# Performance work log

Measured on AMD Instinct MI355X. Metric: run time of the kernel, lower is better.

## Reference

```python
import math
import jax, jax.numpy as jnp
import numpy as np

D_MODEL = 1024
NUM_HEADS = 16
D_K = D_MODEL // NUM_HEADS
RANK = 16
B, L = 2, 2048


def setup_inputs() -> dict:
    key = jax.random.key(0)
    ks = jax.random.split(key, 10)
    w_scale = 0.02  # keep activations well-scaled like trained linears
    return {
        "x_q": jax.random.normal(ks[0], (B, L, D_MODEL), jnp.float32),
        "x_kv": jax.random.normal(ks[1], (B, L, D_MODEL), jnp.float32),
        "Wq": jax.random.normal(ks[2], (D_MODEL, D_MODEL), jnp.float32) * w_scale,
        "bq": jnp.zeros((D_MODEL,), jnp.float32),
        "Wk": jax.random.normal(ks[3], (D_MODEL, D_MODEL), jnp.float32) * w_scale,
        "bk": jnp.zeros((D_MODEL,), jnp.float32),
        "Wv": jax.random.normal(ks[4], (D_MODEL, D_MODEL), jnp.float32) * w_scale,
        "bv": jnp.zeros((D_MODEL,), jnp.float32),
        "Wo": jax.random.normal(ks[5], (D_MODEL, D_MODEL), jnp.float32) * w_scale,
        "bo": jnp.zeros((D_MODEL,), jnp.float32),
        "U_bil": jax.random.normal(ks[6], (NUM_HEADS, D_K, RANK), jnp.float32) * 0.02,
        "V_bil": jax.random.normal(ks[7], (NUM_HEADS, D_K, RANK), jnp.float32) * 0.02,
        "padding_mask": jnp.zeros((B, L), bool),  # True = padded KV position
    }


def reference(x_q, x_kv, Wq, bq, Wk, bk, Wv, bv, Wo, bo, U_bil, V_bil, padding_mask):
    b, l, _ = x_q.shape
    # torch nn.Linear: y = x @ W.T + b
    Q = (x_q @ Wq.T + bq).reshape(b, l, NUM_HEADS, D_K).transpose(0, 2, 1, 3)  # [B,H,L,dk]
    K = (x_kv @ Wk.T + bk).reshape(b, l, NUM_HEADS, D_K).transpose(0, 2, 1, 3)
    V = (x_kv @ Wv.T + bv).reshape(b, l, NUM_HEADS, D_K).transpose(0, 2, 1, 3)
    # low-rank bilinear projections: [B,H,L,rank]
    Q_proj = jnp.einsum("bhld,hdr->bhlr", Q, U_bil)
    K_proj = jnp.einsum("bhld,hdr->bhlr", K, V_bil)
    scores = jnp.einsum("bhqr,bhkr->bhqk", Q_proj, K_proj) / math.sqrt(RANK)  # [B,H,L,L]
    scores = jnp.where(padding_mask[:, None, None, :], jnp.float32(-10000.0), scores)
    attn = jax.nn.softmax(scores, axis=-1)  # dropout is identity in eval mode
    ctx = jnp.einsum("bhqk,bhkd->bhqd", attn, V)
    ctx = ctx.transpose(0, 2, 1, 3).reshape(b, l, D_MODEL)
    return ctx @ Wo.T + bo
```

## Files before the change

kernel.cpp:

```cpp
#include <hip/hip_runtime.h>
#include <hip/hip_bf16.h>

#define DM   1024
#define NH   16
#define DK   64
#define RK   16
#define BB   2
#define LL   2048
#define TT   (BB*LL)
#define HRK  256
#define NSPL 2


typedef float f4   __attribute__((ext_vector_type(4)));
typedef float f16v __attribute__((ext_vector_type(16)));
typedef short s8v  __attribute__((ext_vector_type(8)));
typedef unsigned int u2v __attribute__((ext_vector_type(2)));
typedef unsigned int u4v __attribute__((ext_vector_type(4)));

static __device__ __forceinline__ unsigned short f2b(float f) {
  __hip_bfloat16 h = __float2bfloat16(f);
  unsigned short u;
  __builtin_memcpy(&u, &h, 2);
  return u;
}
static __device__ __forceinline__ float b2f(unsigned short u) {
  __hip_bfloat16 h;
  __builtin_memcpy(&h, &u, 2);
  return __bfloat162float(h);
}

__global__ __launch_bounds__(256) void cast_all(
    const float* __restrict__ s0, unsigned short* __restrict__ d0, int n0,
    const float* __restrict__ s1, unsigned short* __restrict__ d1, int n1,
    const float* __restrict__ s2, unsigned short* __restrict__ d2, int n2,
    const float* __restrict__ s3, unsigned short* __restrict__ d3, int n3) {
  const float* s; unsigned short* d; int n;
  switch (blockIdx.y) {
    case 0:  s = s0; d = d0; n = n0; break;
    case 1:  s = s1; d = d1; n = n1; break;
    case 2:  s = s2; d = d2; n = n2; break;
    default: s = s3; d = d3; n = n3; break;
  }
  for (int i = blockIdx.x*256 + threadIdx.x; i < n; i += gridDim.x*256) {
    const float4 v = ((const float4*)s)[i];
    ushort4 o;
    o.x = f2b(v.x); o.y = f2b(v.y); o.z = f2b(v.z); o.w = f2b(v.w);
    ((ushort4*)d)[i] = o;
  }
}

__global__ __launch_bounds__(256) void fuse_w(
    const float* __restrict__ Wq, const float* __restrict__ Wk,
    const float* __restrict__ Uq, const float* __restrict__ Uk,
    unsigned short* __restrict__ Aq, unsigned short* __restrict__ Ak) {
  const float* W = blockIdx.z ? Wk : Wq;
  const float* U = blockIdx.z ? Uk : Uq;
  unsigned short* At = blockIdx.z ? Ak : Aq;
  __shared__ float Us[64][16];
  __shared__ float Ws[4][64];
  const int i0 = blockIdx.x * 64;
  const int h  = blockIdx.y;
  const int tid = threadIdx.x;
  const int il = tid & 63, rr = tid >> 6;
  for (int t = tid; t < 64*16; t += 256)
    Us[t >> 4][t & 15] = U[(size_t)(h*DK + (t >> 4))*RK + (t & 15)];
  float acc[4] = {};
  for (int d0 = 0; d0 < DK; d0 += 4) {
    __syncthreads();
    Ws[rr][il] = W[(size_t)(h*DK + d0 + rr)*DM + i0 + il];
    __syncthreads();
#pragma unroll
    for (int dd = 0; dd < 4; ++dd) {
      const float w = Ws[dd][il];
#pragma unroll
      for (int j = 0; j < 4; ++j)
        acc[j] += w * Us[d0 + dd][rr*4 + j];
    }
  }
#pragma unroll
  for (int j = 0; j < 4; ++j)
    At[(size_t)(h*RK + rr*4 + j)*DM + i0 + il] = f2b(acc[j]);
}

__global__ void bias2(const float* __restrict__ bq, const float* __restrict__ bk,
                      const float* __restrict__ Uq, const float* __restrict__ Uk,
                      float* __restrict__ bpq, float* __restrict__ bpk) {
  const int t = threadIdx.x;
  const float* b = (t < 256) ? bq : bk;
  const float* U = (t < 256) ? Uq : Uk;
  float* bp = (t < 256) ? bpq : bpk;
  const int hr = t & 255, h = hr >> 4, r = hr & 15;
  float acc = 0.f;
  for (int d = 0; d < DK; ++d)
    acc += b[h*DK + d] * U[(size_t)(h*DK + d)*RK + r];
  bp[hr] = acc;
}

__global__ __launch_bounds__(256) void vsum_k(
    const unsigned short* __restrict__ Vt, float* __restrict__ Vsum) {
  const int h = blockIdx.x, b = blockIdx.y;
  const int d = threadIdx.x >> 2, part = threadIdx.x & 3;
  const unsigned short* row = Vt + ((size_t)b*DM + h*DK + d)*LL + part*512;
  float s = 0.f;
  for (int i = 0; i < 512; i += 8) {
    const s8v v = *(const s8v*)&row[i];
#pragma unroll
    for (int j = 0; j < 8; ++j) s += b2f((unsigned short)v[j]);
  }
  s += __shfl_xor(s, 1);
  s += __shfl_xor(s, 2);
  if (part == 0) Vsum[((size_t)b*NH + h)*DK + d] = s;
}

template<int N_, int MODE, int AF32>
__global__ __launch_bounds__(256) void gemm64(
    const void* __restrict__ A0, const void* __restrict__ A1,
    const unsigned short* __restrict__ B0, const unsigned short* __restrict__ B1,
    const float* __restrict__ bi0, const float* __restrict__ bi1,
    void* __restrict__ C0, void* __restrict__ C1) {
  const void* Agv = blockIdx.z ? A1 : A0;
  const unsigned short* Bg = blockIdx.z ? B1 : B0;
  const float* bias = blockIdx.z ? bi1 : bi0;
  void* Cgv = blockIdx.z ? C1 : C0;
  __shared__ unsigned short Xs[64*40];
  __shared__ unsigned short Bs[128*40];
  const int t0 = blockIdx.x * 64, n0 = blockIdx.y * 128;
  const int tid = threadIdx.x, wave = tid >> 6, lane = tid & 63;
  const int quad = lane >> 4, l15 = lane & 15;
  const int nh = wave * 32;

  const f4 z = {0.f, 0.f, 0.f, 0.f};
  f4 acc[4][2];
#pragma unroll
  for (int a = 0; a < 4; ++a) { acc[a][0] = z; acc[a][1] = z; }

  for (int k0 = 0; k0 < DM; k0 += 32) {
    __syncthreads();
    {
      const int ar = tid >> 2, ap = tid & 3;
      if (AF32) {
        const float* Af = (const float*)Agv;
        const float4 x0 = *(const float4*)&Af[(size_t)(t0 + ar)*DM + k0 + ap*8];
        const float4 x1 = *(const float4*)&Af[(size_t)(t0 + ar)*DM + k0 + ap*8 + 4];
        s8v v;
        v[0]=(short)f2b(x0.x); v[1]=(short)f2b(x0.y);
        v[2]=(short)f2b(x0.z); v[3]=(short)f2b(x0.w);
        v[4]=(short)f2b(x1.x); v[5]=(short)f2b(x1.y);
        v[6]=(short)f2b(x1.z); v[7]=(short)f2b(x1.w);
        *(s8v*)&Xs[ar*40 + ap*8] = v;
      } else {
        *(s8v*)&Xs[ar*40 + ap*8] =
            *(const s8v*)&((const unsigned short*)Agv)[(size_t)(t0 + ar)*DM + k0 + ap*8];
      }
      const int br = tid >> 1, bp = tid & 1;
      *(s8v*)&Bs[br*40 + bp*16] =
          *(const s8v*)&Bg[(size_t)(n0 + br)*DM + k0 + bp*16];
      *(s8v*)&Bs[br*40 + bp*16 + 8] =
          *(const s8v*)&Bg[(size_t)(n0 + br)*DM + k0 + bp*16 + 8];
    }
    __syncthreads();

    s8v af[4], bf[2];
#pragma unroll
    for (int ms = 0; ms < 4; ++ms)
      af[ms] = *(const s8v*)&Xs[(ms*16 + l15)*40 + quad*8];
#pragma unroll
    for (int ns = 0; ns < 2; ++ns)
      bf[ns] = *(const s8v*)&Bs[(nh + ns*16 + l15)*40 + quad*8];
#pragma unroll
    for (int ms = 0; ms < 4; ++ms)
#pragma unroll
      for (int ns = 0; ns < 2; ++ns)
        acc[ms][ns] = __builtin_amdgcn_mfma_f32_16x16x32_bf16(
            af[ms], bf[ns], acc[ms][ns], 0, 0, 0);
  }

#pragma unroll
  for (int ms = 0; ms < 4; ++ms) {
    const int tb = t0 + ms*16 + quad*4;
#pragma unroll
    for (int ns = 0; ns < 2; ++ns) {
      const int o = n0 + nh + ns*16 + l15;
      const float bv = bias[o];
      f4 a = acc[ms][ns];
      if (MODE == 0) {
        float* C = (float*)Cgv;
#pragma unroll
        for (int rg = 0; rg < 4; ++rg)
          C[(size_t)(tb + rg)*N_ + o] = a[rg] + bv;
      } else if (MODE == 1) {
        unsigned short* C = (unsigned short*)Cgv;
#pragma unroll
        for (int rg = 0; rg < 4; ++rg) {
          const int tt = tb + rg;
          C[(((size_t)(tt >> 11)*NH + (o >> 4))*LL + (tt & 2047))*RK + (o & 15)]
              = f2b(a[rg] + bv);
        }
      } else {
        unsigned short* C = (unsigned short*)Cgv;
        const int bb = tb >> 11, l = tb & 2047;
        ushort4 pk;
        pk.x = f2b(a[0] + bv); pk.y = f2b(a[1] + bv);
        pk.z = f2b(a[2] + bv); pk.w = f2b(a[3] + bv);
        *(ushort4*)&C[((size_t)bb*DM + o)*LL + l] = pk;
      }
    }
  }
}

template<bool MASKED>
static __device__ __forceinline__ void softmax_pack(
    const f16v& s0, const f16v& s1, const unsigned long long mb, const int hi,
    float& den, unsigned int (&Pd)[2][4][2]) {
#pragma unroll
  for (int nt = 0; nt < 2; ++nt) {
    const f16v& sv = nt ? s1 : s0;
#pragma unroll
    for (int r = 0; r < 4; ++r) {
      float ep[4];
#pragma unroll
      for (int j = 0; j < 4; ++j) {
        float em = __expf(sv[r*4 + j] * 0.25f);
        if (MASKED) {
          const int kloc = nt*32 + j + 8*r + 4*hi;
          if ((mb >> kloc) & 1ull) em = 0.f;
        }
        den += em;
        ep[j] = em - 1.f;
      }
      asm("v_cvt_pk_bf16_f32 %0, %1, %2"
          : "=v"(Pd[nt][r][0]) : "v"(ep[0]), "v"(ep[1]));
      asm("v_cvt_pk_bf16_f32 %0, %1, %2"
          : "=v"(Pd[nt][r][1]) : "v"(ep[2]), "v"(ep[3]));
    }
  }
}

__global__ __launch_bounds__(256) void attention_v8(
    const unsigned short* __restrict__ Qp, const unsigned short* __restrict__ Kp,
    const unsigned short* __restrict__ Vt,
    const unsigned char* __restrict__ msk,
    unsigned short* __restrict__ P, float* __restrict__ denP) {
  __shared__ __align__(16) unsigned short Ks[2][2][64][8];
  __shared__ __align__(16) unsigned short Vs[2][8][64][8];
  const int q0 = blockIdx.x * 128, h = blockIdx.y;
  const int b = blockIdx.z & (BB - 1), ksp = blockIdx.z >> 1;
  const int kbeg = ksp * (LL / NSPL);
  const int NT = (LL / NSPL) / 64;
  const int tid = threadIdx.x, w = tid >> 6, lane = tid & 63;
  const int l31 = lane & 31, hi = lane >> 5;

  const s8v qfrag = *(const s8v*)&Qp[
      (((size_t)b*NH + h)*LL + q0 + w*32 + l31)*RK + hi*8];

  const int sr = tid >> 2, sp = tid & 3;
  const unsigned short* __restrict__ Vrow =
      Vt + ((size_t)b*DM + h*DK + sr)*LL + kbeg;
  const unsigned short* __restrict__ Kbase =
      Kp + (((size_t)b*NH + h)*LL + kbeg + sr)*RK + sp*4;
  const unsigned char*  __restrict__ Mrow = msk + (size_t)b*LL + kbeg + lane;

  u2v kpre; s8v vpre0, vpre1;
  unsigned char mcur, mnext;

  kpre  = *(const u2v*)&Kbase[0];
  vpre0 = *(const s8v*)&Vrow[sp*16];
  vpre1 = *(const s8v*)&Vrow[sp*16 + 8];
  mcur  = Mrow[0];
  *(u2v*)&Ks[0][sp>>1][sr][(sp&1)*4] = kpre;
  *(s8v*)&Vs[0][sp*2][sr][0]   = vpre0;
  *(s8v*)&Vs[0][sp*2+1][sr][0] = vpre1;
  kpre  = *(const u2v*)&Kbase[(size_t)64*RK];
  vpre0 = *(const s8v*)&Vrow[64 + sp*16];
  vpre1 = *(const s8v*)&Vrow[64 + sp*16 + 8];
  mnext = Mrow[64];
  __syncthreads();

  f16v acc0, acc1, z16;
#pragma unroll
  for (int i = 0; i < 16; ++i) { acc0[i] = 0.f; acc1[i] = 0.f; z16[i] = 0.f; }
  float den = 0.f;

  for (int t = 0; t < NT; ++t) {
    const int cur = t & 1;
    const unsigned long long mb = __ballot(mcur != 0);

    const s8v kf0 = *(const s8v*)&Ks[cur][hi][l31][0];
    const s8v kf1 = *(const s8v*)&Ks[cur][hi][32 + l31][0];

    const f16v s0 = __builtin_amdgcn_mfma_f32_32x32x16_bf16(kf0, qfrag, z16, 0, 0, 0);
    const f16v s1 = __builtin_amdgcn_mfma_f32_32x32x16_bf16(kf1, qfrag, z16, 0, 0, 0);

    unsigned int Pd[2][4][2];
    if (__builtin_expect(mb != 0ull, 0))
      softmax_pack<true >(s0, s1, mb, hi, den, Pd);
    else
      softmax_pack<false>(s0, s1, mb, hi, den, Pd);

#pragma unroll
    for (int kc = 0; kc < 4; ++kc) {
      const int nt = kc >> 1, a = (kc & 1)*2;
      const u2v r0 = __builtin_amdgcn_permlane32_swap(
          Pd[nt][a][0], Pd[nt][a+1][0], false, false);
      const u2v r1 = __builtin_amdgcn_permlane32_swap(
          Pd[nt][a][1], Pd[nt][a+1][1], false, false);
      u4v efi;
      efi[0] = r0[0];
      efi[1] = r1[0];
      efi[2] = r0[1];
      efi[3] = r1[1];
      const s8v ef = __builtin_bit_cast(s8v, efi);
      const s8v vf0 = *(const s8v*)&Vs[cur][kc*2 + hi][l31][0];
      const s8v vf1 = *(const s8v*)&Vs[cur][kc*2 + hi][32 + l31][0];
      acc0 = __builtin_amdgcn_mfma_f32_32x32x16_bf16(ef, vf0, acc0, 0, 0, 0);
      acc1 = __builtin_amdgcn_mfma_f32_32x32x16_bf16(ef, vf1, acc1, 0, 0, 0);
    }

    if (t + 1 < NT) {
      *(u2v*)&Ks[cur^1][sp>>1][sr][(sp&1)*4] = kpre;
      *(s8v*)&Vs[cur^1][sp*2][sr][0]   = vpre0;
      *(s8v*)&Vs[cur^1][sp*2+1][sr][0] = vpre1;
      const int tn = (t + 2 < NT) ? t + 2 : NT - 1;
      kpre  = *(const u2v*)&Kbase[(size_t)tn*64*RK];
      vpre0 = *(const s8v*)&Vrow[tn*64 + sp*16];
      vpre1 = *(const s8v*)&Vrow[tn*64 + sp*16 + 8];
      mcur  = mnext;
      mnext = Mrow[tn*64];
    }
    __syncthreads();
  }

  den += __shfl_xor(den, 32);
  if (hi == 0)
    denP[(((size_t)ksp*BB + b)*NH + h)*LL + q0 + w*32 + l31] = den;

#pragma unroll
  for (int rg = 0; rg < 16; ++rg) {
    const int qr = (rg & 3) + 8*(rg >> 2) + 4*hi;
    const size_t base = 2*(((size_t)(b*LL + q0 + w*32 + qr))*DM + h*DK) + ksp;
    P[base + 2*l31]        = f2b(acc0[rg]);
    P[base + 2*(32 + l31)] = f2b(acc1[rg]);
  }
}

__global__ __launch_bounds__(256) void reduce_k(
    unsigned int* __restrict__ P, const float* __restrict__ Vsum,
    const float* __restrict__ denP) {
  const size_t j0 = ((size_t)blockIdx.x*256 + threadIdx.x)*4;
  const int t  = (int)(j0 >> 10);
  const int dm = (int)(j0 & 1023);
  const int b = t >> 11, l = t & 2047;
  const int h = dm >> 6, d = dm & 63;
  const float dn =
      denP[((size_t)b*NH + h)*LL + l] +
      denP[(((size_t)BB + b)*NH + h)*LL + l];
  const float inv = 1.f / fmaxf(dn, 1e-30f);
  const f4 vs = *(const f4*)&Vsum[((size_t)b*NH + h)*DK + d];
  const u4v p = *(const u4v*)&P[j0];
  f4 c;
#pragma unroll
  for (int i = 0; i < 4; ++i)
    c[i] = (vs[i] + b2f((unsigned short)(p[i] & 0xffff))
                  + b2f((unsigned short)(p[i] >> 16))) * inv;
  *(f4*)&P[j0] = c;
}

extern "C" void kernel_launch(void* const* d_in, const int* in_sizes, int n_in,
                              void* d_out, int out_size, void* d_ws, size_t ws_size,
                              hipStream_t stream) {
  (void)in_sizes; (void)n_in; (void)out_size; (void)ws_size;
  const float* x_q   = (const float*)d_in[0];
  const float* x_kv  = (const float*)d_in[1];
  const float* Wq    = (const float*)d_in[2];
  const float* bq    = (const float*)d_in[3];
  const float* Wk    = (const float*)d_in[4];
  const float* bk    = (const float*)d_in[5];
  const float* Wv    = (const float*)d_in[6];
  const float* bv    = (const float*)d_in[7];
  const float* Wo    = (const float*)d_in[8];
  const float* bo    = (const float*)d_in[9];
  const float* U_bil = (const float*)d_in[10];
  const float* V_bil = (const float*)d_in[11];
  const unsigned char* pmask = (const unsigned char*)d_in[12];
  float* out = (float*)d_out;

  char* w = (char*)d_ws;
  unsigned short* xq_b  = (unsigned short*)(w);
  unsigned short* xkv_b = (unsigned short*)(w +  8388608);
  unsigned short* Wv_b  = (unsigned short*)(w + 16777216);
  unsigned short* Wo_b  = (unsigned short*)(w + 18874368);
  unsigned short* Atq   = (unsigned short*)(w + 20971520);
  unsigned short* Atk   = (unsigned short*)(w + 21495808);
  float*          bpq   = (float*)(w + 22020096);
  float*          bpk   = (float*)(w + 22021120);
  unsigned short* Qp    = (unsigned short*)(w + 22022144);
  unsigned short* Kp    = (unsigned short*)(w + 24119296);
  unsigned short* Vt    = (unsigned short*)(w + 26216448);
  float*          Vsum  = (float*)(w + 34605056);
  float*          denP  = (float*)(w + 34613248);
  unsigned short* Pbuf  = (unsigned short*)w;
  float*          ctx   = (float*)w;

  cast_all<<<dim3(1024, 4), 256, 0, stream>>>(
      x_q, xq_b, TT*DM/4, x_kv, xkv_b, TT*DM/4,
      Wv, Wv_b, DM*DM/4,  Wo, Wo_b, DM*DM/4);
  fuse_w<<<dim3(DM/64, NH, 2), 256, 0, stream>>>(Wq, Wk, U_bil, V_bil, Atq, Atk);
  bias2<<<1, 512, 0, stream>>>(bq, bk, U_bil, V_bil, bpq, bpk);
  gemm64<HRK, 1, 0><<<dim3(64, 2, 2), 256, 0, stream>>>(
      xq_b, xkv_b, Atq, Atk, bpq, bpk, Qp, Kp);
  gemm64<DM, 2, 0><<<dim3(64, 8, 1), 256, 0, stream>>>(
      xkv_b, xkv_b, Wv_b, Wv_b, bv, bv, Vt, Vt);
  vsum_k<<<dim3(NH, BB), 256, 0, stream>>>(Vt, Vsum);
  attention_v8<<<dim3(LL/128, NH, BB*NSPL), 256, 0, stream>>>(
      Qp, Kp, Vt, pmask, Pbuf, denP);
  reduce_k<<<dim3(TT*DM/1024), 256, 0, stream>>>((unsigned int*)w, Vsum, denP);
  gemm64<DM, 0, 1><<<dim3(64, 8, 1), 256, 0, stream>>>(
      ctx, ctx, Wo_b, Wo_b, bo, bo, out, out);
}
```

Baseline: 267.8 us.

## Use direct global-to-LDS loads in GEMM and emit bf16 context from reduce

The GEMM tile loads now go through global_load_lds, which writes straight into shared memory without staging through registers. The LDS row padding is removed, so tiles are unpadded with a 32-element stride. The reduce kernel now writes the context as bf16 into the freed Vt buffer, so the output projection reads bf16 and no longer converts fp32 on load. This halves the context traffic and removes the fp32 A path, but the unpadded LDS layout may cause bank conflicts, and the context loses precision.

```diff
diff --git a/kernel.cpp b/kernel.cpp
--- a/kernel.cpp
+++ b/kernel.cpp
@@ -28,6 +28,12 @@
   __hip_bfloat16 h;
   __builtin_memcpy(&h, &u, 2);
   return __bfloat162float(h);
+}
+
+static __device__ __forceinline__ void gld_lds16(const void* g, void* l) {
+  __builtin_amdgcn_global_load_lds(
+      (const __attribute__((address_space(1))) unsigned int*)g,
+      (__attribute__((address_space(3))) unsigned int*)l, 16, 0, 0);
 }
 
 __global__ __launch_bounds__(256) void cast_all(
@@ -113,22 +119,23 @@
   if (part == 0) Vsum[((size_t)b*NH + h)*DK + d] = s;
 }
 
-template<int N_, int MODE, int AF32>
+template<int N_, int MODE>
 __global__ __launch_bounds__(256) void gemm64(
-    const void* __restrict__ A0, const void* __restrict__ A1,
+    const unsigned short* __restrict__ A0, const unsigned short* __restrict__ A1,
     const unsigned short* __restrict__ B0, const unsigned short* __restrict__ B1,
     const float* __restrict__ bi0, const float* __restrict__ bi1,
     void* __restrict__ C0, void* __restrict__ C1) {
-  const void* Agv = blockIdx.z ? A1 : A0;
+  const unsigned short* Ag = blockIdx.z ? A1 : A0;
   const unsigned short* Bg = blockIdx.z ? B1 : B0;
   const float* bias = blockIdx.z ? bi1 : bi0;
   void* Cgv = blockIdx.z ? C1 : C0;
-  __shared__ unsigned short Xs[64*40];
-  __shared__ unsigned short Bs[128*40];
+  __shared__ __align__(16) unsigned short Xs[64*32];
+  __shared__ __align__(16) unsigned short Bs[128*32];
   const int t0 = blockIdx.x * 64, n0 = blockIdx.y * 128;
   const int tid = threadIdx.x, wave = tid >> 6, lane = tid & 63;
   const int quad = lane >> 4, l15 = lane & 15;
   const int nh = wave * 32;
+  const int ar = tid >> 2, ac = (tid & 3) * 8;
 
   const f4 z = {0.f, 0.f, 0.f, 0.f};
   f4 acc[4][2];
@@ -137,37 +144,18 @@
 
   for (int k0 = 0; k0 < DM; k0 += 32) {
     __syncthreads();
-    {
-      const int ar = tid >> 2, ap = tid & 3;
-      if (AF32) {
-        const float* Af = (const float*)Agv;
-        const float4 x0 = *(const float4*)&Af[(size_t)(t0 + ar)*DM + k0 + ap*8];
-        const float4 x1 = *(const float4*)&Af[(size_t)(t0 + ar)*DM + k0 + ap*8 + 4];
-        s8v v;
-        v[0]=(short)f2b(x0.x); v[1]=(short)f2b(x0.y);
-        v[2]=(short)f2b(x0.z); v[3]=(short)f2b(x0.w);
-        v[4]=(short)f2b(x1.x); v[5]=(short)f2b(x1.y);
-        v[6]=(short)f2b(x1.z); v[7]=(short)f2b(x1.w);
-        *(s8v*)&Xs[ar*40 + ap*8] = v;
-      } else {
-        *(s8v*)&Xs[ar*40 + ap*8] =
-            *(const s8v*)&((const unsigned short*)Agv)[(size_t)(t0 + ar)*DM + k0 + ap*8];
-      }
-      const int br = tid >> 1, bp = tid & 1;
-      *(s8v*)&Bs[br*40 + bp*16] =
-          *(const s8v*)&Bg[(size_t)(n0 + br)*DM + k0 + bp*16];
-      *(s8v*)&Bs[br*40 + bp*16 + 8] =
-          *(const s8v*)&Bg[(size_t)(n0 + br)*DM + k0 + bp*16 + 8];
-    }
+    gld_lds16(&Ag[(size_t)(t0 + ar)*DM + k0 + ac],       &Xs[wave*512]);
+    gld_lds16(&Bg[(size_t)(n0 + ar)*DM + k0 + ac],       &Bs[wave*512]);
+    gld_lds16(&Bg[(size_t)(n0 + 64 + ar)*DM + k0 + ac],  &Bs[2048 + wave*512]);
     __syncthreads();
 
     s8v af[4], bf[2];
 #pragma unroll
     for (int ms = 0; ms < 4; ++ms)
-      af[ms] = *(const s8v*)&Xs[(ms*16 + l15)*40 + quad*8];
+      af[ms] = *(const s8v*)&Xs[(ms*16 + l15)*32 + quad*8];
 #pragma unroll
     for (int ns = 0; ns < 2; ++ns)
-      bf[ns] = *(const s8v*)&Bs[(nh + ns*16 + l15)*40 + quad*8];
+      bf[ns] = *(const s8v*)&Bs[(nh + ns*16 + l15)*32 + quad*8];
 #pragma unroll
     for (int ms = 0; ms < 4; ++ms)
 #pragma unroll
@@ -345,8 +333,8 @@
 }
 
 __global__ __launch_bounds__(256) void reduce_k(
-    unsigned int* __restrict__ P, const float* __restrict__ Vsum,
-    const float* __restrict__ denP) {
+    const unsigned int* __restrict__ P, const float* __restrict__ Vsum,
+    const float* __restrict__ denP, unsigned short* __restrict__ ctxb) {
   const size_t j0 = ((size_t)blockIdx.x*256 + threadIdx.x)*4;
   const int t  = (int)(j0 >> 10);
   const int dm = (int)(j0 & 1023);
@@ -358,12 +346,17 @@
   const float inv = 1.f / fmaxf(dn, 1e-30f);
   const f4 vs = *(const f4*)&Vsum[((size_t)b*NH + h)*DK + d];
   const u4v p = *(const u4v*)&P[j0];
-  f4 c;
-#pragma unroll
-  for (int i = 0; i < 4; ++i)
-    c[i] = (vs[i] + b2f((unsigned short)(p[i] & 0xffff))
-                  + b2f((unsigned short)(p[i] >> 16))) * inv;
-  *(f4*)&P[j0] = c;
+  ushort4 pk;
+  float c0 = (vs[0] + b2f((unsigned short)(p[0] & 0xffff))
+                    + b2f((unsigned short)(p[0] >> 16))) * inv;
+  float c1 = (vs[1] + b2f((unsigned short)(p[1] & 0xffff))
+                    + b2f((unsigned short)(p[1] >> 16))) * inv;
+  float c2 = (vs[2] + b2f((unsigned short)(p[2] & 0xffff))
+                    + b2f((unsigned short)(p[2] >> 16))) * inv;
+  float c3 = (vs[3] + b2f((unsigned short)(p[3] & 0xffff))
+                    + b2f((unsigned short)(p[3] >> 16))) * inv;
+  pk.x = f2b(c0); pk.y = f2b(c1); pk.z = f2b(c2); pk.w = f2b(c3);
+  *(ushort4*)&ctxb[j0] = pk;
 }
 
 extern "C" void kernel_launch(void* const* d_in, const int* in_sizes, int n_in,
@@ -400,21 +393,22 @@
   float*          Vsum  = (float*)(w + 34605056);
   float*          denP  = (float*)(w + 34613248);
   unsigned short* Pbuf  = (unsigned short*)w;
-  float*          ctx   = (float*)w;
+  unsigned short* ctxb  = Vt;
 
   cast_all<<<dim3(1024, 4), 256, 0, stream>>>(
       x_q, xq_b, TT*DM/4, x_kv, xkv_b, TT*DM/4,
       Wv, Wv_b, DM*DM/4,  Wo, Wo_b, DM*DM/4);
   fuse_w<<<dim3(DM/64, NH, 2), 256, 0, stream>>>(Wq, Wk, U_bil, V_bil, Atq, Atk);
   bias2<<<1, 512, 0, stream>>>(bq, bk, U_bil, V_bil, bpq, bpk);
-  gemm64<HRK, 1, 0><<<dim3(64, 2, 2), 256, 0, stream>>>(
+  gemm64<HRK, 1><<<dim3(64, 2, 2), 256, 0, stream>>>(
       xq_b, xkv_b, Atq, Atk, bpq, bpk, Qp, Kp);
-  gemm64<DM, 2, 0><<<dim3(64, 8, 1), 256, 0, stream>>>(
+  gemm64<DM, 2><<<dim3(64, 8, 1), 256, 0, stream>>>(
       xkv_b, xkv_b, Wv_b, Wv_b, bv, bv, Vt, Vt);
   vsum_k<<<dim3(NH, BB), 256, 0, stream>>>(Vt, Vsum);
   attention_v8<<<dim3(LL/128, NH, BB*NSPL), 256, 0, stream>>>(
       Qp, Kp, Vt, pmask, Pbuf, denP);
-  reduce_k<<<dim3(TT*DM/1024), 256, 0, stream>>>((unsigned int*)w, Vsum, denP);
-  gemm64<DM, 0, 1><<<dim3(64, 8, 1), 256, 0, stream>>>(
-      ctx, ctx, Wo_b, Wo_b, bo, bo, out, out);
-}
+  reduce_k<<<dim3(TT*DM/1024), 256, 0, stream>>>(
+      (const unsigned int*)w, Vsum, denP, ctxb);
+  gemm64<DM, 0><<<dim3(64, 8, 1), 256, 0, stream>>>(
+      ctxb, ctxb, Wo_b, Wo_b, bo, bo, out, out);
+}
```

New measurement: 251.5 us. -6.1%, faster.
